# Performance work log

Measured on AMD Instinct MI355X. Metric: run time of the kernel, lower is better.

## Reference

```python
import jax, jax.numpy as jnp
import numpy as np

NUM_HEADS = 12
HEAD_DIM = 64
HIDDEN = 768
BATCH = 2
SEQ = 2048
NEG_BIG = 1e12


def _rope_tables(seq_len, dim, dtype=jnp.float32):
    # theta_i = 10000^(-2i/dim); sin/cos repeat-interleaved -> [seq_len, dim]
    half = dim // 2
    theta = jnp.power(10000.0, -jnp.arange(half, dtype=dtype) * (2.0 / dim))
    ang = jnp.arange(seq_len, dtype=dtype)[:, None] * theta[None, :]  # [n, half]
    sin_pos = jnp.repeat(jnp.sin(ang), 2, axis=-1)  # [n, dim]
    cos_pos = jnp.repeat(jnp.cos(ang), 2, axis=-1)
    return sin_pos, cos_pos


def setup_inputs() -> dict:
    key = jax.random.key(0)
    k1, k2, k3, k4 = jax.random.split(key, 4)
    inputs = jax.random.normal(k1, (BATCH, SEQ, HIDDEN), dtype=jnp.float32)
    mask = jax.random.randint(k2, (BATCH, SEQ), 0, 2, dtype=jnp.int32)
    # nn.Linear(hidden, num_heads*head_dim*2): weight [out, in], bias [out]
    W = jax.random.normal(k3, (NUM_HEADS * HEAD_DIM * 2, HIDDEN), dtype=jnp.float32) * (HIDDEN ** -0.5)
    b = jax.random.normal(k4, (NUM_HEADS * HEAD_DIM * 2,), dtype=jnp.float32) * 0.02
    return {"inputs": inputs, "mask": mask, "W": W, "b": b}


def reference(inputs, mask, W, b):
    B, N, _ = inputs.shape
    H, D = NUM_HEADS, HEAD_DIM
    hs = jnp.einsum('bnh,oh->bno', inputs, W) + b          # [B, N, 2*H*D]
    hs = hs.reshape(B, N, H, 2 * D)                        # split+stack -> [B, N, H, 2D]
    qw, kw = hs[..., :D], hs[..., D:]                      # [B, N, H, D]
    # qw2 = cat([-q_odd, q_even], -1) as in the torch code
    qw2 = jnp.concatenate([-qw[..., 1::2], qw[..., ::2]], axis=-1)
    kw2 = jnp.concatenate([-kw[..., 1::2], kw[..., ::2]], axis=-1)
    # permute to [B, H, N, D]
    qw, qw2 = qw.transpose(0, 2, 1, 3), qw2.transpose(0, 2, 1, 3)
    kw, kw2 = kw.transpose(0, 2, 1, 3), kw2.transpose(0, 2, 1, 3)
    sin_pos, cos_pos = _rope_tables(N, D, hs.dtype)        # [N, D], broadcasts over B, H
    qw = qw * cos_pos + qw2 * sin_pos
    kw = kw * cos_pos + kw2 * sin_pos
    logits = jnp.einsum('bhnd,bhmd->bhnm', qw, kw)         # [B, H, N, N]
    # padding mask over key axis: mask [B,N] -> [B,1,1,N]
    pad = mask.astype(logits.dtype)[:, None, None, :]
    logits = logits * pad - (1.0 - pad) * NEG_BIG
    # strictly-lower-triangular mask (keep upper triangle + diagonal)
    tril = jnp.tril(jnp.ones((N, N), dtype=logits.dtype), k=-1)
    logits = logits - tril * NEG_BIG
    return logits / (D ** 0.5)
```

## Files before the change

kernel.cpp:

```cpp
#include <hip/hip_runtime.h>
#include <hip/hip_bf16.h>
#include <cmath>

#define NH   12
#define HD   64
#define HID  768
#define NB   2
#define SEQL 2048
#define ROWS 4096
#define OUTW 1536

static constexpr float NEGBIG = 1000000000000.0f;

typedef __attribute__((ext_vector_type(4)))  float f32x4;
typedef __attribute__((ext_vector_type(8)))  short short8;
typedef __attribute__((ext_vector_type(16))) float f32x16;

__device__ __forceinline__ unsigned short f2bf(float f) {
    unsigned int u = __builtin_bit_cast(unsigned int, f);
    u += 0x7FFFu + ((u >> 16) & 1u);
    return (unsigned short)(u >> 16);
}

__device__ __forceinline__ short8 cvt8(const float* __restrict__ p) {
    float4 v0 = *reinterpret_cast<const float4*>(p);
    float4 v1 = *reinterpret_cast<const float4*>(p + 4);
    short8 g;
    g[0] = (short)f2bf(v0.x); g[1] = (short)f2bf(v0.y);
    g[2] = (short)f2bf(v0.z); g[3] = (short)f2bf(v0.w);
    g[4] = (short)f2bf(v1.x); g[5] = (short)f2bf(v1.y);
    g[6] = (short)f2bf(v1.z); g[7] = (short)f2bf(v1.w);
    return g;
}

__device__ __forceinline__ void fill_tile(int fid, int tid,
                                          const int* __restrict__ mask,
                                          float* __restrict__ out) {
    const int bh = fid / 120;
    int j = fid % 120;
    int ntv = 1;
    while (j >= ntv) { j -= ntv; ++ntv; }
    const int nt = ntv, mt = j;
    const int bI = bh / NH;
    float* outbase = out + (size_t)bh * SEQL * SEQL;
    const int cg = tid & 31;
    const int r0 = tid >> 5;
    const int m0 = mt * 128 + cg * 4;
    const int4 mi = *reinterpret_cast<const int4*>(mask + bI * SEQL + m0);
    f32x4 v;
    v.x = ((float)mi.x - 2.0f) * (NEGBIG * 0.125f);
    v.y = ((float)mi.y - 2.0f) * (NEGBIG * 0.125f);
    v.z = ((float)mi.z - 2.0f) * (NEGBIG * 0.125f);
    v.w = ((float)mi.w - 2.0f) * (NEGBIG * 0.125f);
    float* ob = outbase + (size_t)(nt * 128) * SEQL + m0;
#pragma unroll
    for (int jj = 0; jj < 16; ++jj) {
        int row = r0 + 8 * jj;
        __builtin_nontemporal_store(v, reinterpret_cast<f32x4*>(ob + (size_t)row * SEQL));
    }
}

#define WQ (OUTW * HID / 4)
#define RQ (SEQL * 32)
#define PREP_BLOCKS 1408
#define FILL_PREP   700
#define FILL_P1     2180
__global__ void k_prep(const float* __restrict__ W,
                       unsigned short* __restrict__ Wbf, float2* __restrict__ rtab,
                       const int* __restrict__ mask, float* __restrict__ out) {
    if (blockIdx.x >= PREP_BLOCKS) {
        fill_tile(blockIdx.x - PREP_BLOCKS, threadIdx.x, mask, out);
        return;
    }
    int i = blockIdx.x * blockDim.x + threadIdx.x;
    if (i < WQ) {
        float4 v = reinterpret_cast<const float4*>(W)[i];
        ushort4 o;
        o.x = f2bf(v.x); o.y = f2bf(v.y); o.z = f2bf(v.z); o.w = f2bf(v.w);
        reinterpret_cast<ushort4*>(Wbf)[i] = o;
    } else if (i < WQ + RQ) {
        int idx = i - WQ;
        int n = idx >> 5, d = idx & 31;
        float theta = exp2f(-(float)d * (13.287712379549449f / 32.0f));
        float ang = (float)n * theta;
        rtab[idx] = make_float2(sinf(ang), cosf(ang));
    }
}

__global__ __launch_bounds__(256, 4) void k_proj_fill(
    const float* __restrict__ X,
    const unsigned short* __restrict__ Wbf,
    const float*  __restrict__ bias,
    const float2* __restrict__ rtab,
    unsigned short* __restrict__ Qbf,
    unsigned short* __restrict__ Kbf,
    const int* __restrict__ mask,
    float* __restrict__ out)
{
    const int bid = blockIdx.x;
    const int tid = threadIdx.x;

    if (bid >= 768) {
        fill_tile(FILL_PREP + (bid - 768), tid, mask, out);
        return;
    }

    const int newbid = (bid & 7) * 96 + (bid >> 3);
    const int slab = newbid / 12;
    const int head = newbid % 12;
    const int row0 = slab * 64;
    const int lane = tid & 63;
    const int w    = tid >> 6;
    const int wr = w & 1, wc = w >> 1;
    const int l31 = lane & 31, lhi = lane >> 5;
    const int x7  = l31 & 7;

    __shared__ __align__(16) unsigned short smem[12288];

    f32x16 acc[2];
    {
        float bj0 = bias[head * 128 + wc * 64 + l31];
        float bj1 = bias[head * 128 + wc * 64 + 32 + l31];
#pragma unroll
        for (int r = 0; r < 16; ++r) { acc[0][r] = bj0; acc[1][r] = bj1; }
    }

    const float* Abase = X + (size_t)row0 * HID;
    const unsigned short* Bbase = Wbf + (size_t)(head * 128) * HID;

    short8 ga[2], gb[4];
#pragma unroll
    for (int r = 0; r < 2; ++r) {
        int idx = tid + 256 * r, row = idx >> 3, s = idx & 7;
        ga[r] = cvt8(Abase + (size_t)row * HID + s * 8);
    }
#pragma unroll
    for (int r = 0; r < 4; ++r) {
        int idx = tid + 256 * r, row = idx >> 3, s = idx & 7;
        gb[r] = *reinterpret_cast<const short8*>(Bbase + (size_t)row * HID + s * 8);
    }
#pragma unroll
    for (int r = 0; r < 2; ++r) {
        int idx = tid + 256 * r, row = idx >> 3, s = idx & 7, ws = s ^ (row & 7);
        *reinterpret_cast<short8*>(smem + row * 64 + ws * 8) = ga[r];
    }
#pragma unroll
    for (int r = 0; r < 4; ++r) {
        int idx = tid + 256 * r, row = idx >> 3, s = idx & 7, ws = s ^ (row & 7);
        *reinterpret_cast<short8*>(smem + 4096 + row * 64 + ws * 8) = gb[r];
    }

    for (int t = 0; t < 12; ++t) {
        __syncthreads();
        if (t < 11) {
            const int kk = (t + 1) * 64;
#pragma unroll
            for (int r = 0; r < 2; ++r) {
                int idx = tid + 256 * r, row = idx >> 3, s = idx & 7;
                ga[r] = cvt8(Abase + (size_t)row * HID + kk + s * 8);
            }
#pragma unroll
            for (int r = 0; r < 4; ++r) {
                int idx = tid + 256 * r, row = idx >> 3, s = idx & 7;
                gb[r] = *reinterpret_cast<const short8*>(Bbase + (size_t)row * HID + kk + s * 8);
            }
        }
#pragma unroll
        for (int ks = 0; ks < 4; ++ks) {
            int sl = (ks * 2 + lhi) ^ x7;
            short8 a  = *reinterpret_cast<const short8*>(smem + (wr * 32 + l31) * 64 + sl * 8);
            short8 b0 = *reinterpret_cast<const short8*>(smem + 4096 + (wc * 64 + l31) * 64 + sl * 8);
            short8 b1 = *reinterpret_cast<const short8*>(smem + 4096 + (wc * 64 + 32 + l31) * 64 + sl * 8);
            acc[0] = __builtin_amdgcn_mfma_f32_32x32x16_bf16(a, b0, acc[0], 0, 0, 0);
            acc[1] = __builtin_amdgcn_mfma_f32_32x32x16_bf16(a, b1, acc[1], 0, 0, 0);
        }
        if (t < 11) {
            __syncthreads();
#pragma unroll
            for (int r = 0; r < 2; ++r) {
                int idx = tid + 256 * r, row = idx >> 3, s = idx & 7, ws = s ^ (row & 7);
                *reinterpret_cast<short8*>(smem + row * 64 + ws * 8) = ga[r];
            }
#pragma unroll
            for (int r = 0; r < 4; ++r) {
                int idx = tid + 256 * r, row = idx >> 3, s = idx & 7, ws = s ^ (row & 7);
                *reinterpret_cast<short8*>(smem + 4096 + row * 64 + ws * 8) = gb[r];
            }
        }
    }
    __syncthreads();

    float (*hs)[132] = reinterpret_cast<float (*)[132]>(smem);
    for (int s = 0; s < 2; ++s) {
        if (wr == s) {
#pragma unroll
            for (int j = 0; j < 2; ++j)
#pragma unroll
                for (int r = 0; r < 16; ++r) {
                    int rr = (r & 3) + 8 * (r >> 2) + 4 * lhi;
                    hs[rr][wc * 64 + j * 32 + l31] = acc[j][r];
                }
        }
        __syncthreads();
#pragma unroll 4
        for (int it = 0; it < 8; ++it) {
            int f   = tid + 256 * it;
            int row = f >> 6;
            int u   = f & 63;
            int isK = u >> 5;
            int dp  = u & 31;
            int d0  = 2 * dp, d1 = d0 + 1;
            int cb  = isK * 64;
            int grow = row0 + s * 32 + row;
            int bI = grow >> 11;
            int n  = grow & 2047;
            float2 sc = rtab[n * 32 + dp];
            float v0 = hs[row][cb + d0];
            float v1 = hs[row][cb + d1];
            int p0 = (d0 < 32) ? (2 * d0 + 1) : (2 * d0 - 64);
            int p1 = (d1 < 32) ? (2 * d1 + 1) : (2 * d1 - 64);
            float pv0 = hs[row][cb + p0];
            float pv1 = hs[row][cb + p1];
            float sg0 = (d0 < 32) ? -1.0f : 1.0f;
            float sg1 = (d1 < 32) ? -1.0f : 1.0f;
            ushort2 st;
            st.x = f2bf(v0 * sc.y + sg0 * pv0 * sc.x);
            st.y = f2bf(v1 * sc.y + sg1 * pv1 * sc.x);
            unsigned short* dst = isK ? (unsigned short*)Kbf : (unsigned short*)Qbf;
            size_t idx = ((size_t)(bI * NH + head) * SEQL + n) * HD + d0;
            *reinterpret_cast<ushort2*>(dst + idx) = st;
        }
        __syncthreads();
    }
}

__global__ __launch_bounds__(256) void k_logits(
    const unsigned short* __restrict__ Qbf,
    const unsigned short* __restrict__ Kbf,
    const int* __restrict__ mask,
    float* __restrict__ out)
{
    const int bid = blockIdx.x;
    const int newbid = (bid & 7) * 408 + (bid >> 3);
    const int tid = threadIdx.x;

    const int bh = newbid / 136;
    int j = newbid % 136;
    int ntv = 0;
    while (j >= 16 - ntv) { j -= 16 - ntv; ++ntv; }
    const int nt = ntv, mt = ntv + j;
    const int bI = bh / NH;
    float* outbase = out + (size_t)bh * SEQL * SEQL;

    const int lane = tid & 63;
    const int w = tid >> 6;
    const int rowHalf = w & 1, colHalf = w >> 1;
    const int l31 = lane & 31, lhi = lane >> 5;
    const int n0 = nt * 128 + rowHalf * 64;
    const int m0 = mt * 128 + colHalf * 64;

    f32x16 acc[2][2];
#pragma unroll
    for (int i = 0; i < 2; ++i)
#pragma unroll
        for (int jj = 0; jj < 2; ++jj)
#pragma unroll
            for (int r = 0; r < 16; ++r) acc[i][jj][r] = 0.0f;

    const unsigned short* Aq = Qbf + ((size_t)bh * SEQL + n0 + l31) * HD + 8 * lhi;
    const unsigned short* Bk = Kbf + ((size_t)bh * SEQL + m0 + l31) * HD + 8 * lhi;
#pragma unroll
    for (int t2 = 0; t2 < 4; ++t2) {
        short8 a0 = *reinterpret_cast<const short8*>(Aq + 16 * t2);
        short8 a1 = *reinterpret_cast<const short8*>(Aq + 32 * HD + 16 * t2);
        short8 b0 = *reinterpret_cast<const short8*>(Bk + 16 * t2);
        short8 b1 = *reinterpret_cast<const short8*>(Bk + 32 * HD + 16 * t2);
        acc[0][0] = __builtin_amdgcn_mfma_f32_32x32x16_bf16(a0, b0, acc[0][0], 0, 0, 0);
        acc[0][1] = __builtin_amdgcn_mfma_f32_32x32x16_bf16(a0, b1, acc[0][1], 0, 0, 0);
        acc[1][0] = __builtin_amdgcn_mfma_f32_32x32x16_bf16(a1, b0, acc[1][0], 0, 0, 0);
        acc[1][1] = __builtin_amdgcn_mfma_f32_32x32x16_bf16(a1, b1, acc[1][1], 0, 0, 0);
    }

    __shared__ float tl[64][128];
#pragma unroll
    for (int i = 0; i < 2; ++i) {
#pragma unroll
        for (int jj = 0; jj < 2; ++jj) {
#pragma unroll
            for (int r = 0; r < 16; ++r) {
                int rr = (r & 3) + 8 * (r >> 2) + 4 * lhi;
                tl[rowHalf * 32 + rr][colHalf * 64 + jj * 32 + l31] = acc[i][jj][r];
            }
        }
        __syncthreads();
#pragma unroll
        for (int it = 0; it < 8; ++it) {
            int f   = tid + 256 * it;
            int lr  = f >> 5;
            int cg  = f & 31;
            int grow = nt * 128 + (lr >> 5) * 64 + i * 32 + (lr & 31);
            int gcol = mt * 128 + cg * 4;
            const int4 mi = *reinterpret_cast<const int4*>(mask + bI * SEQL + gcol);
            f32x4 v = *reinterpret_cast<const f32x4*>(&tl[lr][cg * 4]);
            float pads[4] = {(float)mi.x, (float)mi.y, (float)mi.z, (float)mi.w};
#pragma unroll
            for (int e = 0; e < 4; ++e) {
                float vv = v[e] * pads[e] - (1.0f - pads[e]) * NEGBIG;
                if (gcol + e < grow) vv -= NEGBIG;
                v[e] = vv * 0.125f;
            }
            __builtin_nontemporal_store(v, reinterpret_cast<f32x4*>(outbase + (size_t)grow * SEQL + gcol));
        }
        __syncthreads();
    }
}

extern "C" void kernel_launch(void* const* d_in, const int* in_sizes, int n_in,
                              void* d_out, int out_size, void* d_ws, size_t ws_size,
                              hipStream_t stream) {
    const float* x    = (const float*)d_in[0];
    const int*   mask = (const int*)d_in[1];
    const float* W    = (const float*)d_in[2];
    const float* bias = (const float*)d_in[3];
    float* out = (float*)d_out;

    char* ws = (char*)d_ws;
    unsigned short* Wbf = (unsigned short*)(ws);
    unsigned short* Qbf = (unsigned short*)(ws + 2359296);
    unsigned short* Kbf = (unsigned short*)(ws + 8650752);
    float2*         rtab = (float2*)(ws + 14942208);

    k_prep<<<dim3(PREP_BLOCKS + FILL_PREP), dim3(256), 0, stream>>>(W, Wbf, rtab, mask, out);
    k_proj_fill<<<dim3(768 + FILL_P1), dim3(256), 0, stream>>>(x, Wbf, bias, rtab, Qbf, Kbf, mask, out);
    k_logits<<<dim3(3264), dim3(256), 0, stream>>>(Qbf, Kbf, mask, out);
}
```

Before: 89.97 us.

## Fuse W bf16 conversion into projection, double-buffer LDS, spread fill tiles

```diff
diff --git a/kernel.cpp b/kernel.cpp
--- a/kernel.cpp
+++ b/kernel.cpp
@@ -60,36 +60,27 @@
     }
 }
 
-#define WQ (OUTW * HID / 4)
 #define RQ (SEQL * 32)
-#define PREP_BLOCKS 1408
-#define FILL_PREP   700
-#define FILL_P1     2180
-__global__ void k_prep(const float* __restrict__ W,
-                       unsigned short* __restrict__ Wbf, float2* __restrict__ rtab,
+#define PREP_BLOCKS 256
+#define FILL_PREP   900
+#define FILL_P1     1396
+#define FILL_P2     584
+__global__ void k_prep(float2* __restrict__ rtab,
                        const int* __restrict__ mask, float* __restrict__ out) {
     if (blockIdx.x >= PREP_BLOCKS) {
         fill_tile(blockIdx.x - PREP_BLOCKS, threadIdx.x, mask, out);
         return;
     }
-    int i = blockIdx.x * blockDim.x + threadIdx.x;
-    if (i < WQ) {
-        float4 v = reinterpret_cast<const float4*>(W)[i];
-        ushort4 o;
-        o.x = f2bf(v.x); o.y = f2bf(v.y); o.z = f2bf(v.z); o.w = f2bf(v.w);
-        reinterpret_cast<ushort4*>(Wbf)[i] = o;
-    } else if (i < WQ + RQ) {
-        int idx = i - WQ;
-        int n = idx >> 5, d = idx & 31;
-        float theta = exp2f(-(float)d * (13.287712379549449f / 32.0f));
-        float ang = (float)n * theta;
-        rtab[idx] = make_float2(sinf(ang), cosf(ang));
-    }
-}
-
-__global__ __launch_bounds__(256, 4) void k_proj_fill(
+    int idx = blockIdx.x * blockDim.x + threadIdx.x;
+    int n = idx >> 5, d = idx & 31;
+    float theta = exp2f(-(float)d * (13.287712379549449f / 32.0f));
+    float ang = (float)n * theta;
+    rtab[idx] = make_float2(sinf(ang), cosf(ang));
+}
+
+__global__ __launch_bounds__(256, 3) void k_proj_fill(
     const float* __restrict__ X,
-    const unsigned short* __restrict__ Wbf,
+    const float* __restrict__ W,
     const float*  __restrict__ bias,
     const float2* __restrict__ rtab,
     unsigned short* __restrict__ Qbf,
@@ -115,7 +106,7 @@
     const int l31 = lane & 31, lhi = lane >> 5;
     const int x7  = l31 & 7;
 
-    __shared__ __align__(16) unsigned short smem[12288];
+    __shared__ __align__(16) unsigned short smem[24576];
 
     f32x16 acc[2];
     {
@@ -126,7 +117,7 @@
     }
 
     const float* Abase = X + (size_t)row0 * HID;
-    const unsigned short* Bbase = Wbf + (size_t)(head * 128) * HID;
+    const float* Bbase = W + (size_t)(head * 128) * HID;
 
     short8 ga[2], gb[4];
 #pragma unroll
@@ -137,7 +128,7 @@
 #pragma unroll
     for (int r = 0; r < 4; ++r) {
         int idx = tid + 256 * r, row = idx >> 3, s = idx & 7;
-        gb[r] = *reinterpret_cast<const short8*>(Bbase + (size_t)row * HID + s * 8);
+        gb[r] = cvt8(Bbase + (size_t)row * HID + s * 8);
     }
 #pragma unroll
     for (int r = 0; r < 2; ++r) {
@@ -147,11 +138,12 @@
 #pragma unroll
     for (int r = 0; r < 4; ++r) {
         int idx = tid + 256 * r, row = idx >> 3, s = idx & 7, ws = s ^ (row & 7);
-        *reinterpret_cast<short8*>(smem + 4096 + row * 64 + ws * 8) = gb[r];
-    }
+        *reinterpret_cast<short8*>(smem + 8192 + row * 64 + ws * 8) = gb[r];
+    }
+    __syncthreads();
 
     for (int t = 0; t < 12; ++t) {
-        __syncthreads();
+        const int cur = t & 1;
         if (t < 11) {
             const int kk = (t + 1) * 64;
 #pragma unroll
@@ -162,33 +154,35 @@
 #pragma unroll
             for (int r = 0; r < 4; ++r) {
                 int idx = tid + 256 * r, row = idx >> 3, s = idx & 7;
-                gb[r] = *reinterpret_cast<const short8*>(Bbase + (size_t)row * HID + kk + s * 8);
-            }
-        }
+                gb[r] = cvt8(Bbase + (size_t)row * HID + kk + s * 8);
+            }
+        }
+        const unsigned short* Ab = smem + cur * 4096;
+        const unsigned short* Bb = smem + 8192 + cur * 8192;
 #pragma unroll
         for (int ks = 0; ks < 4; ++ks) {
             int sl = (ks * 2 + lhi) ^ x7;
-            short8 a  = *reinterpret_cast<const short8*>(smem + (wr * 32 + l31) * 64 + sl * 8);
-            short8 b0 = *reinterpret_cast<const short8*>(smem + 4096 + (wc * 64 + l31) * 64 + sl * 8);
-            short8 b1 = *reinterpret_cast<const short8*>(smem + 4096 + (wc * 64 + 32 + l31) * 64 + sl * 8);
+            short8 a  = *reinterpret_cast<const short8*>(Ab + (wr * 32 + l31) * 64 + sl * 8);
+            short8 b0 = *reinterpret_cast<const short8*>(Bb + (wc * 64 + l31) * 64 + sl * 8);
+            short8 b1 = *reinterpret_cast<const short8*>(Bb + (wc * 64 + 32 + l31) * 64 + sl * 8);
             acc[0] = __builtin_amdgcn_mfma_f32_32x32x16_bf16(a, b0, acc[0], 0, 0, 0);
             acc[1] = __builtin_amdgcn_mfma_f32_32x32x16_bf16(a, b1, acc[1], 0, 0, 0);
         }
         if (t < 11) {
-            __syncthreads();
+            const int nxt = cur ^ 1;
 #pragma unroll
             for (int r = 0; r < 2; ++r) {
                 int idx = tid + 256 * r, row = idx >> 3, s = idx & 7, ws = s ^ (row & 7);
-                *reinterpret_cast<short8*>(smem + row * 64 + ws * 8) = ga[r];
+                *reinterpret_cast<short8*>(smem + nxt * 4096 + row * 64 + ws * 8) = ga[r];
             }
 #pragma unroll
             for (int r = 0; r < 4; ++r) {
                 int idx = tid + 256 * r, row = idx >> 3, s = idx & 7, ws = s ^ (row & 7);
-                *reinterpret_cast<short8*>(smem + 4096 + row * 64 + ws * 8) = gb[r];
-            }
-        }
-    }
-    __syncthreads();
+                *reinterpret_cast<short8*>(smem + 8192 + nxt * 8192 + row * 64 + ws * 8) = gb[r];
+            }
+        }
+        __syncthreads();
+    }
 
     float (*hs)[132] = reinterpret_cast<float (*)[132]>(smem);
     for (int s = 0; s < 2; ++s) {
@@ -241,8 +235,13 @@
     float* __restrict__ out)
 {
     const int bid = blockIdx.x;
-    const int newbid = (bid & 7) * 408 + (bid >> 3);
+    const int newbid = (bid & 7) * 481 + (bid >> 3);
     const int tid = threadIdx.x;
+
+    if (newbid >= 3264) {
+        fill_tile(FILL_PREP + FILL_P1 + (newbid - 3264), tid, mask, out);
+        return;
+    }
 
     const int bh = newbid / 136;
     int j = newbid % 136;
@@ -325,12 +324,11 @@
     float* out = (float*)d_out;
 
     char* ws = (char*)d_ws;
-    unsigned short* Wbf = (unsigned short*)(ws);
-    unsigned short* Qbf = (unsigned short*)(ws + 2359296);
-    unsigned short* Kbf = (unsigned short*)(ws + 8650752);
-    float2*         rtab = (float2*)(ws + 14942208);
-
-    k_prep<<<dim3(PREP_BLOCKS + FILL_PREP), dim3(256), 0, stream>>>(W, Wbf, rtab, mask, out);
-    k_proj_fill<<<dim3(768 + FILL_P1), dim3(256), 0, stream>>>(x, Wbf, bias, rtab, Qbf, Kbf, mask, out);
-    k_logits<<<dim3(3264), dim3(256), 0, stream>>>(Qbf, Kbf, mask, out);
-}
+    unsigned short* Qbf = (unsigned short*)(ws);
+    unsigned short* Kbf = (unsigned short*)(ws + 6291456);
+    float2*         rtab = (float2*)(ws + 12582912);
+
+    k_prep<<<dim3(PREP_BLOCKS + FILL_PREP), dim3(256), 0, stream>>>(rtab, mask, out);
+    k_proj_fill<<<dim3(768 + FILL_P1), dim3(256), 0, stream>>>(x, W, bias, rtab, Qbf, Kbf, mask, out);
+    k_logits<<<dim3(3848), dim3(256), 0, stream>>>(Qbf, Kbf, mask, out);
+}
```

After: 113.2 us. 25.8% more time.
